# Performance work log

Hardware: AMD Instinct MI355X
Metric: run time of the kernel (lower is better)

Reference implementation:

```python
import jax, jax.numpy as jnp
import numpy as np

H = 4096
NH = 32
HD = 128
FF = 14336
EPS = 1e-6


def _rmsnorm(x, w):
    xf = x.astype(jnp.float32)
    var = jnp.mean(xf * xf, axis=-1, keepdims=True)
    return (w * (xf * jax.lax.rsqrt(var + EPS))).astype(x.dtype)


def setup_inputs() -> dict:
    key = jax.random.key(0)
    ks = jax.random.split(key, 16)
    S = 2048
    def lin(k, fan_in, shape):
        bound = 1.0 / np.sqrt(fan_in)
        return jax.random.uniform(k, shape, jnp.float32, -bound, bound)
    return {
        "hidden_states": jax.random.normal(ks[0], (S, H), jnp.float32),
        "position_ids": jnp.arange(S, dtype=jnp.int64),
        "wq": lin(ks[1], H, (NH * HD, H)), "bq": lin(ks[2], H, (NH * HD,)),
        "wk": lin(ks[3], H, (NH * HD, H)), "bk": lin(ks[4], H, (NH * HD,)),
        "wv": lin(ks[5], H, (NH * HD, H)), "bv": lin(ks[6], H, (NH * HD,)),
        "wo": lin(ks[7], H, (H, H)), "bo": lin(ks[8], H, (H,)),
        "w_gate": lin(ks[9], H, (FF, H)),
        "w_up": lin(ks[10], H, (FF, H)),
        "w_down": lin(ks[11], FF, (H, FF)),
        "ln1_w": jnp.ones((H,), jnp.float32),
        "ln2_w": jnp.ones((H,), jnp.float32),
    }


def reference(hidden_states, position_ids, wq, bq, wk, bk, wv, bv, wo, bo,
              w_gate, w_up, w_down, ln1_w, ln2_w):
    S = hidden_states.shape[0]
    # --- attention block ---
    x = _rmsnorm(hidden_states, ln1_w)
    q = (x @ wq.T + bq).reshape(S, NH, HD)
    k = (x @ wk.T + bk).reshape(S, NH, HD)
    v = (x @ wv.T + bv).reshape(S, NH, HD)
    scale = 1.0 / np.sqrt(HD)
    scores = jnp.einsum('qhd,khd->hqk', q.astype(jnp.float32),
                        k.astype(jnp.float32)) * scale
    causal = jnp.tril(jnp.ones((S, S), bool))  # decoder causal mask
    scores = jnp.where(causal[None, :, :], scores, -jnp.inf)
    probs = jax.nn.softmax(scores, axis=-1)
    h = jnp.einsum('hqk,khd->qhd', probs, v.astype(jnp.float32))
    attn_out = h.reshape(S, NH * HD).astype(hidden_states.dtype) @ wo.T + bo
    h1 = hidden_states + attn_out
    # --- SwiGLU MLP block ---
    y = _rmsnorm(h1, ln2_w)
    mlp = (jax.nn.silu(y @ w_gate.T) * (y @ w_up.T)) @ w_down.T
    return h1 + mlp
```

## Files before the change

kernel.cpp:

```cpp
#include <hip/hip_runtime.h>
#include <math.h>

#define H_DIM 4096
#define NHEAD 32
#define HD 128
#define FF_DIM 14336

typedef unsigned short u16;
typedef __attribute__((ext_vector_type(8))) short bf16x8;
typedef __attribute__((ext_vector_type(4))) float f32x4;
typedef __attribute__((ext_vector_type(4))) unsigned short u16x4;

typedef const __attribute__((address_space(1))) void* gas_ptr;
typedef __attribute__((address_space(3))) void* las_ptr;

__device__ __forceinline__ void gload_lds16(const void* g, void* l) {
  __builtin_amdgcn_global_load_lds((gas_ptr)g, (las_ptr)l, 16, 0, 0);
}

__device__ __forceinline__ u16 f32_to_bf16(float f) {
  unsigned int u = __float_as_uint(f);
  u = (u + 0x7FFFu + ((u >> 16) & 1u)) >> 16;
  return (u16)u;
}
__device__ __forceinline__ float bf16_to_f32(u16 x) {
  return __uint_as_float(((unsigned int)x) << 16);
}

__device__ __forceinline__ void conv4(const float* __restrict__ in,
                                      u16* __restrict__ out, long i) {
  const f32x4* p = reinterpret_cast<const f32x4*>(in) + i;
  f32x4 v = __builtin_nontemporal_load(p);
  u16x4 o;
  o.x = f32_to_bf16(v.x); o.y = f32_to_bf16(v.y);
  o.z = f32_to_bf16(v.z); o.w = f32_to_bf16(v.w);
  reinterpret_cast<u16x4*>(out)[i] = o;
}

__global__ void f2b_kernel(const float* __restrict__ in, u16* __restrict__ out, long n4) {
  long i = (long)blockIdx.x * blockDim.x + threadIdx.x;
  long stride = (long)gridDim.x * blockDim.x;
  for (; i < n4; i += stride) conv4(in, out, i);
}

__global__ void f2b3_kernel(const float* __restrict__ a, const float* __restrict__ b,
                            const float* __restrict__ c, u16* __restrict__ out, long n4each) {
  long i = (long)blockIdx.x * blockDim.x + threadIdx.x;
  long st = (long)gridDim.x * blockDim.x;
  long tot = 3 * n4each;
  for (; i < tot; i += st) {
    const float* src; long j;
    if (i < n4each)            { src = a; j = i; }
    else if (i < 2 * n4each)   { src = b; j = i - n4each; }
    else                       { src = c; j = i - 2 * n4each; }
    const f32x4* p = reinterpret_cast<const f32x4*>(src) + j;
    f32x4 v = __builtin_nontemporal_load(p);
    u16x4 o;
    o.x = f32_to_bf16(v.x); o.y = f32_to_bf16(v.y);
    o.z = f32_to_bf16(v.z); o.w = f32_to_bf16(v.w);
    reinterpret_cast<u16x4*>(out)[i] = o;
  }
}

__global__ void bias_concat_kernel(const float* __restrict__ a, const float* __restrict__ b,
                                   const float* __restrict__ c, float* __restrict__ out) {
  int i = blockIdx.x * blockDim.x + threadIdx.x;
  float v;
  if (i < 4096) v = a[i];
  else if (i < 8192) v = b[i - 4096];
  else v = c[i - 8192];
  out[i] = v;
}

__global__ void rmsnorm_kernel(const float* __restrict__ in, const float* __restrict__ w,
                               u16* __restrict__ out) {
  int row = blockIdx.x;
  int tid = threadIdx.x;
  const float4* x4 = reinterpret_cast<const float4*>(in + (size_t)row * H_DIM);
  float4 vv[4];
  float ss = 0.f;
#pragma unroll
  for (int it = 0; it < 4; ++it) {
    float4 v = x4[tid + it * 256];
    vv[it] = v;
    ss += v.x * v.x + v.y * v.y + v.z * v.z + v.w * v.w;
  }
#pragma unroll
  for (int off = 1; off < 64; off <<= 1) ss += __shfl_xor(ss, off);
  __shared__ float part[4];
  if ((tid & 63) == 0) part[tid >> 6] = ss;
  __syncthreads();
  float tot = part[0] + part[1] + part[2] + part[3];
  float rinv = rsqrtf(tot * (1.0f / H_DIM) + 1e-6f);
  const float4* w4 = reinterpret_cast<const float4*>(w);
  u16* orow = out + (size_t)row * H_DIM;
#pragma unroll
  for (int it = 0; it < 4; ++it) {
    float4 v = vv[it];
    float4 wv = w4[tid + it * 256];
    ushort4 o;
    o.x = f32_to_bf16(v.x * rinv * wv.x);
    o.y = f32_to_bf16(v.y * rinv * wv.y);
    o.z = f32_to_bf16(v.z * rinv * wv.z);
    o.w = f32_to_bf16(v.w * rinv * wv.w);
    reinterpret_cast<ushort4*>(orow)[tid + it * 256] = o;
  }
}

enum { EPI_QKV = 0, EPI_O = 1, EPI_SILU = 2, EPI_MUL = 3, EPI_PART = 4 };

template <int EPI, bool SPLIT>
__global__ __launch_bounds__(512, 2) void gemm256(
    const u16* __restrict__ A, const u16* __restrict__ B, void* __restrict__ outp,
    const float* __restrict__ bias, const void* __restrict__ extra,
    int M, int N, int K, int kLen) {
  __shared__ __align__(16) u16 As[2][256 * 64];
  __shared__ __align__(16) u16 Bs[2][256 * 64];
  const int tid = threadIdx.x;
  const int wid = tid >> 6, lane = tid & 63;
  const int lg = lane >> 4, li = lane & 15;
  const int wr = (wid >> 2) << 7;
  const int wc = (wid & 3) << 6;

  const int nbm = M >> 8, nbn = N >> 8;
  const int nb = nbm * nbn;
  int wg = (blockIdx.x & 7) * (gridDim.x >> 3) + (blockIdx.x >> 3);
  int s = 0;
  if (SPLIT) { s = wg / nb; wg -= s * nb; }
  const int m0 = (wg % nbm) << 8, n0 = (wg / nbm) << 8;
  const int kB = SPLIT ? s * kLen : 0;
  const int NT = kLen >> 6;

  const int r8 = tid >> 3;
  const int sl = ((tid & 7) ^ (r8 & 7)) << 3;
  const u16* sA[2][2];
  const u16* sB[2][2];
  int ldo[2][2];
#pragma unroll
  for (int P = 0; P < 2; ++P)
#pragma unroll
    for (int h = 0; h < 2; ++h) {
      int lr = P * 128 + h * 64 + r8;
      int ra = (lr & 63) | ((lr >> 1) & 64) | ((lr << 1) & 128);
      int rb = (lr & 31) | ((lr & 96) << 1) | ((lr & 128) >> 2);
      sA[P][h] = A + (size_t)(m0 + ra) * K + kB + sl;
      sB[P][h] = B + (size_t)(n0 + rb) * K + kB + sl;
      ldo[P][h] = (P * 128 + h * 64 + (wid << 3)) << 6;
    }

  auto stageA = [&](int P, int d, int ko) {
#pragma unroll
    for (int h = 0; h < 2; ++h)
      gload_lds16(sA[P][h] + ko, (void*)(&As[d][ldo[P][h]]));
  };
  auto stageB = [&](int P, int d, int ko) {
#pragma unroll
    for (int h = 0; h < 2; ++h)
      gload_lds16(sB[P][h] + ko, (void*)(&Bs[d][ldo[P][h]]));
  };

  bf16x8 a[4][2], b[4][2];
  f32x4 acc[8][4] = {};
  const int s20 = (lg ^ (li & 7)) << 3;
  const int s21 = ((4 + lg) ^ (li & 7)) << 3;

  auto ldA = [&](int d, int set) {
#pragma unroll
    for (int i = 0; i < 4; ++i) {
      int g = wr + set * 64 + i * 16;
      int lb = (g & 63) | ((g >> 1) & 64) | ((g << 1) & 128);
      const u16* base = &As[d][(lb + li) << 6];
      a[i][0] = *reinterpret_cast<const bf16x8*>(base + s20);
      a[i][1] = *reinterpret_cast<const bf16x8*>(base + s21);
    }
  };
  auto ldB = [&](int d, int set) {
#pragma unroll
    for (int jj = 0; jj < 2; ++jj) {
      int hh = wc + (set * 2 + jj) * 16;
      int lb = ((hh & 32) << 2) | ((hh & 192) >> 1) | (hh & 31);
      const u16* base = &Bs[d][(lb + li) << 6];
      b[set * 2 + jj][0] = *reinterpret_cast<const bf16x8*>(base + s20);
      b[set * 2 + jj][1] = *reinterpret_cast<const bf16x8*>(base + s21);
    }
  };
  auto mm = [&](int iset, int jset) {
    __builtin_amdgcn_s_setprio(1);
#pragma unroll
    for (int i = 0; i < 4; ++i)
#pragma unroll
      for (int jj = 0; jj < 2; ++jj)
#pragma unroll
        for (int kk = 0; kk < 2; ++kk)
          acc[iset * 4 + i][jset * 2 + jj] = __builtin_amdgcn_mfma_f32_16x16x32_bf16(
              a[i][kk], b[jset * 2 + jj][kk], acc[iset * 4 + i][jset * 2 + jj], 0, 0, 0);
    __builtin_amdgcn_s_setprio(0);
  };

  stageA(0, 0, 0); stageB(0, 0, 0); stageB(1, 0, 0); stageA(1, 0, 0);
  if (NT > 1) {
    stageA(0, 1, 64); stageB(0, 1, 64); stageB(1, 1, 64); stageA(1, 1, 64);
    asm volatile("s_waitcnt vmcnt(8)" ::: "memory");
  } else {
    asm volatile("s_waitcnt vmcnt(0)" ::: "memory");
  }
  __builtin_amdgcn_s_barrier();

  for (int t = 0; t < NT; ++t) {
    int d = t & 1;
    bool pf = (t + 2) < NT;
    int ko = (t + 2) << 6;
    ldB(d, 0); ldA(d, 0);
    __builtin_amdgcn_s_barrier();
    mm(0, 0);
    __builtin_amdgcn_s_barrier();
    ldB(d, 1);
    if (pf) { stageA(0, d, ko); stageB(0, d, ko); }
    __builtin_amdgcn_s_barrier();
    mm(0, 1);
    __builtin_amdgcn_s_barrier();
    ldA(d, 1);
    if (pf) stageB(1, d, ko);
    __builtin_amdgcn_s_barrier();
    mm(1, 0);
    __builtin_amdgcn_s_barrier();
    if (pf) {
      stageA(1, d, ko);
      asm volatile("s_waitcnt vmcnt(6)" ::: "memory");
    } else {
      asm volatile("s_waitcnt vmcnt(0)" ::: "memory");
    }
    __builtin_amdgcn_s_barrier();
    mm(1, 1);
    __builtin_amdgcn_s_barrier();
  }

#pragma unroll
  for (int i = 0; i < 8; ++i) {
#pragma unroll
    for (int j = 0; j < 4; ++j) {
      int col = n0 + wc + j * 16 + li;
      float bv = 0.f;
      if (EPI == EPI_QKV || EPI == EPI_O) bv = bias[col];
      if (EPI == EPI_PART && bias != nullptr && s == 0) bv = bias[col];
#pragma unroll
      for (int r = 0; r < 4; ++r) {
        int row = m0 + wr + i * 16 + lg * 4 + r;
        float v = acc[i][j][r] + bv;
        size_t idx = (size_t)row * N + col;
        if (EPI == EPI_QKV) {
          ((u16*)outp)[idx] = f32_to_bf16(v);
        } else if (EPI == EPI_O) {
          const float* res = (const float*)extra;
          ((float*)outp)[idx] = res[idx] + v;
        } else if (EPI == EPI_SILU) {
          float sv = v / (1.f + __expf(-v));
          ((u16*)outp)[idx] = f32_to_bf16(sv);
        } else if (EPI == EPI_MUL) {
          const u16* sg = (const u16*)extra;
          ((u16*)outp)[idx] = f32_to_bf16(v * bf16_to_f32(sg[idx]));
        } else {
          ((float*)outp)[(size_t)s * M * N + idx] = v;
        }
      }
    }
  }
}

__global__ void reduce_down(const float* __restrict__ p, const float* __restrict__ res,
                            float* __restrict__ out, long n4, long str4) {
  long i = (long)blockIdx.x * blockDim.x + threadIdx.x;
  long st = (long)gridDim.x * blockDim.x;
  for (; i < n4; i += st) {
    f32x4 h = reinterpret_cast<const f32x4*>(res)[i];
    f32x4 p0 = __builtin_nontemporal_load(reinterpret_cast<const f32x4*>(p) + i);
    f32x4 p1 = __builtin_nontemporal_load(reinterpret_cast<const f32x4*>(p) + i + str4);
    f32x4 o;
    o.x = h.x + p0.x + p1.x; o.y = h.y + p0.y + p1.y;
    o.z = h.z + p0.z + p1.z; o.w = h.w + p0.w + p1.w;
    __builtin_nontemporal_store(o, reinterpret_cast<f32x4*>(out) + i);
  }
}

__global__ void transpose_kernel(const u16* __restrict__ in, u16* __restrict__ out,
                                 int S, int ldin) {
  __shared__ __align__(16) u16 t[64][80];
  int sbT = S >> 6;
  int bs = blockIdx.x % sbT, bc = blockIdx.x / sbT;
  int s0 = bs << 6, c0 = bc << 6;
  int tid = threadIdx.x;
  int ir = tid >> 3;
  int jc = (tid & 7) * 8;
#pragma unroll
  for (int h = 0; h < 2; ++h) {
    int sr = ir + h * 32;
    uint4 v = *reinterpret_cast<const uint4*>(in + (size_t)(s0 + sr) * ldin + c0 + jc);
    *reinterpret_cast<uint4*>(&t[sr][jc]) = v;
  }
  __syncthreads();
  int d = tid >> 3;
  int ss = (tid & 7) * 8;
#pragma unroll
  for (int h = 0; h < 2; ++h) {
    int dd = d + h * 32;
    u16 tmp[8];
#pragma unroll
    for (int e = 0; e < 8; ++e) tmp[e] = t[ss + e][dd];
    *reinterpret_cast<uint4*>(out + (size_t)(c0 + dd) * S + s0 + ss) =
        *reinterpret_cast<const uint4*>(tmp);
  }
}

__global__ __launch_bounds__(256) void attn_kernel(
    const u16* __restrict__ q, const u16* __restrict__ k,
    const u16* __restrict__ vt, u16* __restrict__ o, int S, int ldqk) {
  __shared__ __align__(16) u16 plds[4][32 * 64];
  int tid = threadIdx.x, wid = tid >> 6, lane = tid & 63;
  int lg = lane >> 4, li = lane & 15;
  int nwg = gridDim.x;
  int sbid = (blockIdx.x & 7) * (nwg >> 3) + (blockIdx.x >> 3);
  int task = sbid * 4 + wid;
  int pairs = S >> 6;
  int head = task / pairs;
  int pi = task - head * pairs;
  const float scale = 0.08838834764831845f;
  u16* pl = plds[wid];

  for (int tix = 0; tix < 2; ++tix) {
    int qt = tix ? ((S >> 5) - 1 - pi) : pi;
    int q0 = qt << 5;

    bf16x8 aq[2][4];
#pragma unroll
    for (int fi = 0; fi < 2; ++fi) {
      const u16* qrow = q + (size_t)(q0 + fi * 16 + li) * ldqk + head * HD + lg * 8;
#pragma unroll
      for (int ks = 0; ks < 4; ++ks)
        aq[fi][ks] = *reinterpret_cast<const bf16x8*>(qrow + ks * 32);
    }

    f32x4 oacc[2][8] = {};
    float m_run[2][4], l_run[2][4];
#pragma unroll
    for (int fi = 0; fi < 2; ++fi)
#pragma unroll
      for (int r = 0; r < 4; ++r) { m_run[fi][r] = -INFINITY; l_run[fi][r] = 0.f; }

    int nkb = ((q0 + 31) >> 6) + 1;
    for (int kb = 0; kb < nkb; ++kb) {
      int kvbase = kb << 6;
      f32x4 sacc[2][4] = {};
#pragma unroll
      for (int cf = 0; cf < 4; ++cf) {
        const u16* krow = k + (size_t)(kvbase + cf * 16 + li) * ldqk + head * HD + lg * 8;
#pragma unroll
        for (int ks = 0; ks < 4; ++ks) {
          bf16x8 bk = *reinterpret_cast<const bf16x8*>(krow + ks * 32);
          sacc[0][cf] = __builtin_amdgcn_mfma_f32_16x16x32_bf16(aq[0][ks], bk, sacc[0][cf], 0, 0, 0);
          sacc[1][cf] = __builtin_amdgcn_mfma_f32_16x16x32_bf16(aq[1][ks], bk, sacc[1][cf], 0, 0, 0);
        }
      }
      bool bnd = (kvbase + 63) > q0;
      float alpha[2][4];
#pragma unroll
      for (int fi = 0; fi < 2; ++fi) {
#pragma unroll
        for (int r = 0; r < 4; ++r) {
          int row = q0 + fi * 16 + lg * 4 + r;
#pragma unroll
          for (int cf = 0; cf < 4; ++cf) {
            float sv = sacc[fi][cf][r] * scale;
            if (bnd && (kvbase + cf * 16 + li) > row) sv = -INFINITY;
            sacc[fi][cf][r] = sv;
          }
          float mv = fmaxf(fmaxf(sacc[fi][0][r], sacc[fi][1][r]),
                           fmaxf(sacc[fi][2][r], sacc[fi][3][r]));
#pragma unroll
          for (int off = 1; off < 16; off <<= 1) mv = fmaxf(mv, __shfl_xor(mv, off));
          float mnew = fmaxf(m_run[fi][r], mv);
          alpha[fi][r] = __expf(m_run[fi][r] - mnew);
          m_run[fi][r] = mnew;
          float ps = 0.f;
#pragma unroll
          for (int cf = 0; cf < 4; ++cf) {
            float pv = __expf(sacc[fi][cf][r] - mnew);
            sacc[fi][cf][r] = pv;
            ps += pv;
          }
#pragma unroll
          for (int off = 1; off < 16; off <<= 1) ps += __shfl_xor(ps, off);
          l_run[fi][r] = l_run[fi][r] * alpha[fi][r] + ps;
        }
      }
#pragma unroll
      for (int fi = 0; fi < 2; ++fi)
#pragma unroll
        for (int df = 0; df < 8; ++df)
#pragma unroll
          for (int r = 0; r < 4; ++r) oacc[fi][df][r] *= alpha[fi][r];
#pragma unroll
      for (int fi = 0; fi < 2; ++fi)
#pragma unroll
        for (int cf = 0; cf < 4; ++cf)
#pragma unroll
          for (int r = 0; r < 4; ++r) {
            int row = fi * 16 + lg * 4 + r;
            int el = row * 64 + cf * 16 + li;
            pl[el ^ ((row & 7) << 3)] = f32_to_bf16(sacc[fi][cf][r]);
          }
      asm volatile("s_waitcnt lgkmcnt(0)" ::: "memory");
      __builtin_amdgcn_sched_barrier(0);
#pragma unroll
      for (int kk = 0; kk < 2; ++kk) {
        bf16x8 pa[2];
#pragma unroll
        for (int fi = 0; fi < 2; ++fi) {
          int row = fi * 16 + li;
          int el = row * 64 + kk * 32 + lg * 8;
          pa[fi] = *reinterpret_cast<const bf16x8*>(pl + (el ^ ((row & 7) << 3)));
        }
        const u16* vb = vt + kvbase + kk * 32 + lg * 8;
#pragma unroll
        for (int df = 0; df < 8; ++df) {
          bf16x8 bv = *reinterpret_cast<const bf16x8*>(vb + (size_t)(head * HD + df * 16 + li) * S);
          oacc[0][df] = __builtin_amdgcn_mfma_f32_16x16x32_bf16(pa[0], bv, oacc[0][df], 0, 0, 0);
          oacc[1][df] = __builtin_amdgcn_mfma_f32_16x16x32_bf16(pa[1], bv, oacc[1][df], 0, 0, 0);
        }
      }
    }
#pragma unroll
    for (int fi = 0; fi < 2; ++fi)
#pragma unroll
      for (int r = 0; r < 4; ++r) {
        float inv = 1.0f / l_run[fi][r];
        int row = q0 + fi * 16 + lg * 4 + r;
        u16* orow = o + (size_t)row * H_DIM + head * HD;
#pragma unroll
        for (int df = 0; df < 8; ++df)
          orow[df * 16 + li] = f32_to_bf16(oacc[fi][df][r] * inv);
      }
  }
}

extern "C" void kernel_launch(void* const* d_in, const int* in_sizes, int n_in,
                              void* d_out, int out_size, void* d_ws, size_t ws_size,
                              hipStream_t stream) {
  (void)n_in; (void)out_size;
  const float* hidden = (const float*)d_in[0];
  const float* wq = (const float*)d_in[2];
  const float* bq = (const float*)d_in[3];
  const float* wk = (const float*)d_in[4];
  const float* bk = (const float*)d_in[5];
  const float* wv = (const float*)d_in[6];
  const float* bv = (const float*)d_in[7];
  const float* wo = (const float*)d_in[8];
  const float* bo = (const float*)d_in[9];
  const float* wg = (const float*)d_in[10];
  const float* wu = (const float*)d_in[11];
  const float* wd = (const float*)d_in[12];
  const float* ln1 = (const float*)d_in[13];
  const float* ln2 = (const float*)d_in[14];
  float* out = (float*)d_out;

  int S = in_sizes[0] / H_DIM;
  int NQKV = 3 * H_DIM;

  char* ws = (char*)d_ws;
  size_t off = 0;
  auto alloc = [&](size_t bytes) {
    void* p = ws + off;
    off += (bytes + 255) & ~(size_t)255;
    return p;
  };
  u16* wbuf = (u16*)alloc((size_t)FF_DIM * H_DIM * 2);
  u16* xb   = (u16*)alloc((size_t)S * H_DIM * 2);
  u16* qkv  = (u16*)alloc((size_t)S * NQKV * 2);
  u16* vtb  = (u16*)alloc((size_t)S * H_DIM * 2);
  u16* hat  = (u16*)alloc((size_t)S * H_DIM * 2);
  float* h1 = (float*)alloc((size_t)S * H_DIM * 4);
  u16* sg   = (u16*)alloc((size_t)S * FF_DIM * 2);
  u16* tb   = (u16*)alloc((size_t)S * FF_DIM * 2);
  float* bcat = (float*)alloc((size_t)NQKV * 4);
  if (off > ws_size) return;
  float* pbuf = (float*)qkv;

  dim3 b256(256), b512(512);
  long nHH4 = (long)H_DIM * H_DIM / 4;
  long nFH4 = (long)FF_DIM * H_DIM / 4;
  int gQKV3 = (S / 256) * (NQKV / 256);
  int gO    = 2 * (S / 256) * (H_DIM / 256);
  int gFF   = (S / 256) * (FF_DIM / 256);
  int gDW   = 2 * (S / 256) * (H_DIM / 256);
  long n4HH = (long)S * H_DIM / 4;
  int gAttn = (NHEAD * (S / 64)) / 4;

  rmsnorm_kernel<<<S, b256, 0, stream>>>(hidden, ln1, xb);
  bias_concat_kernel<<<NQKV / 256, b256, 0, stream>>>(bq, bk, bv, bcat);
  f2b3_kernel<<<4096, b256, 0, stream>>>(wq, wk, wv, wbuf, nHH4);
  gemm256<EPI_QKV, false><<<gQKV3, b512, 0, stream>>>(xb, wbuf, qkv, bcat, nullptr,
                                                      S, NQKV, H_DIM, H_DIM);
  transpose_kernel<<<(S / 64) * (H_DIM / 64), b256, 0, stream>>>(qkv + 2 * H_DIM, vtb, S, NQKV);
  attn_kernel<<<gAttn, b256, 0, stream>>>(qkv, qkv + H_DIM, vtb, hat, S, NQKV);
  f2b_kernel<<<4096, b256, 0, stream>>>(wo, wbuf, nHH4);
  gemm256<EPI_PART, true><<<gO, b512, 0, stream>>>(hat, wbuf, pbuf, bo, nullptr,
                                                   S, H_DIM, H_DIM, H_DIM / 2);
  reduce_down<<<2048, b256, 0, stream>>>(pbuf, hidden, h1, n4HH, n4HH);

  rmsnorm_kernel<<<S, b256, 0, stream>>>(h1, ln2, xb);
  f2b_kernel<<<4096, b256, 0, stream>>>(wg, wbuf, nFH4);
  gemm256<EPI_SILU, false><<<gFF, b512, 0, stream>>>(xb, wbuf, sg, nullptr, nullptr,
                                                     S, FF_DIM, H_DIM, H_DIM);
  f2b_kernel<<<4096, b256, 0, stream>>>(wu, wbuf, nFH4);
  gemm256<EPI_MUL, false><<<gFF, b512, 0, stream>>>(xb, wbuf, tb, nullptr, sg,
                                                    S, FF_DIM, H_DIM, H_DIM);
  f2b_kernel<<<4096, b256, 0, stream>>>(wd, wbuf, nFH4);
  gemm256<EPI_PART, true><<<gDW, b512, 0, stream>>>(tb, wbuf, pbuf, nullptr, nullptr,
                                                    S, H_DIM, FF_DIM, FF_DIM / 2);
  reduce_down<<<2048, b256, 0, stream>>>(pbuf, h1, out, n4HH, n4HH);
}
```

Baseline: 1.520 ms.

## Shrink attention per-wave query tile from 32 to 16 rows for more parallelism

Each attention wave now processes a 16-row query tile instead of two 16-row fragments (32 rows), with tiles still paired front/back for causal load balance. The grid doubles to 512 blocks and per-wave register and LDS use drops. This is meant to raise occupancy and spread the attention work over more waves. In exchange, K and V loads are no longer shared across two query fragments, so global/L2 traffic per useful FLOP doubles, and causal masking now wastes more of each 64-wide KV block.

```diff
diff --git a/kernel.cpp b/kernel.cpp
--- a/kernel.cpp
+++ b/kernel.cpp
@@ -314,131 +314,113 @@
 __global__ __launch_bounds__(256) void attn_kernel(
     const u16* __restrict__ q, const u16* __restrict__ k,
     const u16* __restrict__ vt, u16* __restrict__ o, int S, int ldqk) {
-  __shared__ __align__(16) u16 plds[4][32 * 64];
+  __shared__ __align__(16) u16 plds[4][16 * 64];
   int tid = threadIdx.x, wid = tid >> 6, lane = tid & 63;
   int lg = lane >> 4, li = lane & 15;
   int nwg = gridDim.x;
   int sbid = (blockIdx.x & 7) * (nwg >> 3) + (blockIdx.x >> 3);
   int task = sbid * 4 + wid;
-  int pairs = S >> 6;
+  int pairs = S >> 5;
   int head = task / pairs;
   int pi = task - head * pairs;
   const float scale = 0.08838834764831845f;
   u16* pl = plds[wid];
+  int ntiles = S >> 4;
 
   for (int tix = 0; tix < 2; ++tix) {
-    int qt = tix ? ((S >> 5) - 1 - pi) : pi;
-    int q0 = qt << 5;
-
-    bf16x8 aq[2][4];
-#pragma unroll
-    for (int fi = 0; fi < 2; ++fi) {
-      const u16* qrow = q + (size_t)(q0 + fi * 16 + li) * ldqk + head * HD + lg * 8;
+    int qt = tix ? (ntiles - 1 - pi) : pi;
+    int q0 = qt << 4;
+
+    bf16x8 aq[4];
+    {
+      const u16* qrow = q + (size_t)(q0 + li) * ldqk + head * HD + lg * 8;
 #pragma unroll
       for (int ks = 0; ks < 4; ++ks)
-        aq[fi][ks] = *reinterpret_cast<const bf16x8*>(qrow + ks * 32);
-    }
-
-    f32x4 oacc[2][8] = {};
-    float m_run[2][4], l_run[2][4];
-#pragma unroll
-    for (int fi = 0; fi < 2; ++fi)
-#pragma unroll
-      for (int r = 0; r < 4; ++r) { m_run[fi][r] = -INFINITY; l_run[fi][r] = 0.f; }
-
-    int nkb = ((q0 + 31) >> 6) + 1;
+        aq[ks] = *reinterpret_cast<const bf16x8*>(qrow + ks * 32);
+    }
+
+    f32x4 oacc[8] = {};
+    float m_run[4], l_run[4];
+#pragma unroll
+    for (int r = 0; r < 4; ++r) { m_run[r] = -INFINITY; l_run[r] = 0.f; }
+
+    int nkb = ((q0 + 15) >> 6) + 1;
     for (int kb = 0; kb < nkb; ++kb) {
       int kvbase = kb << 6;
-      f32x4 sacc[2][4] = {};
+      f32x4 sacc[4] = {};
 #pragma unroll
       for (int cf = 0; cf < 4; ++cf) {
         const u16* krow = k + (size_t)(kvbase + cf * 16 + li) * ldqk + head * HD + lg * 8;
 #pragma unroll
         for (int ks = 0; ks < 4; ++ks) {
           bf16x8 bk = *reinterpret_cast<const bf16x8*>(krow + ks * 32);
-          sacc[0][cf] = __builtin_amdgcn_mfma_f32_16x16x32_bf16(aq[0][ks], bk, sacc[0][cf], 0, 0, 0);
-          sacc[1][cf] = __builtin_amdgcn_mfma_f32_16x16x32_bf16(aq[1][ks], bk, sacc[1][cf], 0, 0, 0);
+          sacc[cf] = __builtin_amdgcn_mfma_f32_16x16x32_bf16(aq[ks], bk, sacc[cf], 0, 0, 0);
         }
       }
       bool bnd = (kvbase + 63) > q0;
-      float alpha[2][4];
-#pragma unroll
-      for (int fi = 0; fi < 2; ++fi) {
+      float alpha[4];
+#pragma unroll
+      for (int r = 0; r < 4; ++r) {
+        int row = q0 + lg * 4 + r;
+#pragma unroll
+        for (int cf = 0; cf < 4; ++cf) {
+          float sv = sacc[cf][r] * scale;
+          if (bnd && (kvbase + cf * 16 + li) > row) sv = -INFINITY;
+          sacc[cf][r] = sv;
+        }
+        float mv = fmaxf(fmaxf(sacc[0][r], sacc[1][r]),
+                         fmaxf(sacc[2][r], sacc[3][r]));
+#pragma unroll
+        for (int off = 1; off < 16; off <<= 1) mv = fmaxf(mv, __shfl_xor(mv, off));
+        float mnew = fmaxf(m_run[r], mv);
+        alpha[r] = __expf(m_run[r] - mnew);
+        m_run[r] = mnew;
+        float ps = 0.f;
+#pragma unroll
+        for (int cf = 0; cf < 4; ++cf) {
+          float pv = __expf(sacc[cf][r] - mnew);
+          sacc[cf][r] = pv;
+          ps += pv;
+        }
+#pragma unroll
+        for (int off = 1; off < 16; off <<= 1) ps += __shfl_xor(ps, off);
+        l_run[r] = l_run[r] * alpha[r] + ps;
+      }
+#pragma unroll
+      for (int df = 0; df < 8; ++df)
+#pragma unroll
+        for (int r = 0; r < 4; ++r) oacc[df][r] *= alpha[r];
+#pragma unroll
+      for (int cf = 0; cf < 4; ++cf)
 #pragma unroll
         for (int r = 0; r < 4; ++r) {
-          int row = q0 + fi * 16 + lg * 4 + r;
-#pragma unroll
-          for (int cf = 0; cf < 4; ++cf) {
-            float sv = sacc[fi][cf][r] * scale;
-            if (bnd && (kvbase + cf * 16 + li) > row) sv = -INFINITY;
-            sacc[fi][cf][r] = sv;
-          }
-          float mv = fmaxf(fmaxf(sacc[fi][0][r], sacc[fi][1][r]),
-                           fmaxf(sacc[fi][2][r], sacc[fi][3][r]));
-#pragma unroll
-          for (int off = 1; off < 16; off <<= 1) mv = fmaxf(mv, __shfl_xor(mv, off));
-          float mnew = fmaxf(m_run[fi][r], mv);
-          alpha[fi][r] = __expf(m_run[fi][r] - mnew);
-          m_run[fi][r] = mnew;
-          float ps = 0.f;
-#pragma unroll
-          for (int cf = 0; cf < 4; ++cf) {
-            float pv = __expf(sacc[fi][cf][r] - mnew);
-            sacc[fi][cf][r] = pv;
-            ps += pv;
-          }
-#pragma unroll
-          for (int off = 1; off < 16; off <<= 1) ps += __shfl_xor(ps, off);
-          l_run[fi][r] = l_run[fi][r] * alpha[fi][r] + ps;
+          int row = lg * 4 + r;
+          int el = row * 64 + cf * 16 + li;
+          pl[el ^ ((row & 7) << 3)] = f32_to_bf16(sacc[cf][r]);
+        }
+      asm volatile("s_waitcnt lgkmcnt(0)" ::: "memory");
+      __builtin_amdgcn_sched_barrier(0);
+#pragma unroll
+      for (int kk = 0; kk < 2; ++kk) {
+        int el = li * 64 + kk * 32 + lg * 8;
+        bf16x8 pa = *reinterpret_cast<const bf16x8*>(pl + (el ^ ((li & 7) << 3)));
+        const u16* vb = vt + kvbase + kk * 32 + lg * 8;
+#pragma unroll
+        for (int df = 0; df < 8; ++df) {
+          bf16x8 bv = *reinterpret_cast<const bf16x8*>(vb + (size_t)(head * HD + df * 16 + li) * S);
+          oacc[df] = __builtin_amdgcn_mfma_f32_16x16x32_bf16(pa, bv, oacc[df], 0, 0, 0);
         }
       }
-#pragma unroll
-      for (int fi = 0; fi < 2; ++fi)
-#pragma unroll
-        for (int df = 0; df < 8; ++df)
-#pragma unroll
-          for (int r = 0; r < 4; ++r) oacc[fi][df][r] *= alpha[fi][r];
-#pragma unroll
-      for (int fi = 0; fi < 2; ++fi)
-#pragma unroll
-        for (int cf = 0; cf < 4; ++cf)
-#pragma unroll
-          for (int r = 0; r < 4; ++r) {
-            int row = fi * 16 + lg * 4 + r;
-            int el = row * 64 + cf * 16 + li;
-            pl[el ^ ((row & 7) << 3)] = f32_to_bf16(sacc[fi][cf][r]);
-          }
-      asm volatile("s_waitcnt lgkmcnt(0)" ::: "memory");
-      __builtin_amdgcn_sched_barrier(0);
-#pragma unroll
-      for (int kk = 0; kk < 2; ++kk) {
-        bf16x8 pa[2];
-#pragma unroll
-        for (int fi = 0; fi < 2; ++fi) {
-          int row = fi * 16 + li;
-          int el = row * 64 + kk * 32 + lg * 8;
-          pa[fi] = *reinterpret_cast<const bf16x8*>(pl + (el ^ ((row & 7) << 3)));
-        }
-        const u16* vb = vt + kvbase + kk * 32 + lg * 8;
-#pragma unroll
-        for (int df = 0; df < 8; ++df) {
-          bf16x8 bv = *reinterpret_cast<const bf16x8*>(vb + (size_t)(head * HD + df * 16 + li) * S);
-          oacc[0][df] = __builtin_amdgcn_mfma_f32_16x16x32_bf16(pa[0], bv, oacc[0][df], 0, 0, 0);
-          oacc[1][df] = __builtin_amdgcn_mfma_f32_16x16x32_bf16(pa[1], bv, oacc[1][df], 0, 0, 0);
-        }
-      }
-    }
-#pragma unroll
-    for (int fi = 0; fi < 2; ++fi)
-#pragma unroll
-      for (int r = 0; r < 4; ++r) {
-        float inv = 1.0f / l_run[fi][r];
-        int row = q0 + fi * 16 + lg * 4 + r;
-        u16* orow = o + (size_t)row * H_DIM + head * HD;
-#pragma unroll
-        for (int df = 0; df < 8; ++df)
-          orow[df * 16 + li] = f32_to_bf16(oacc[fi][df][r] * inv);
-      }
+    }
+#pragma unroll
+    for (int r = 0; r < 4; ++r) {
+      float inv = 1.0f / l_run[r];
+      int row = q0 + lg * 4 + r;
+      u16* orow = o + (size_t)row * H_DIM + head * HD;
+#pragma unroll
+      for (int df = 0; df < 8; ++df)
+        orow[df * 16 + li] = f32_to_bf16(oacc[df][r] * inv);
+    }
   }
 }
 
@@ -492,7 +474,7 @@
   int gFF   = (S / 256) * (FF_DIM / 256);
   int gDW   = 2 * (S / 256) * (H_DIM / 256);
   long n4HH = (long)S * H_DIM / 4;
-  int gAttn = (NHEAD * (S / 64)) / 4;
+  int gAttn = (NHEAD * (S / 16)) / 2 / 4;
 
   rmsnorm_kernel<<<S, b256, 0, stream>>>(hidden, ln1, xb);
   bias_concat_kernel<<<NQKV / 256, b256, 0, stream>>>(bq, bk, bv, bcat);
```

Measured after the change: 1.481 ms. 2.6% less time.
